# Performance work log

Hardware: AMD Instinct MI355X
Metric: run time of the kernel (lower is better)

Reference implementation:

```python
import jax, jax.numpy as jnp
import numpy as np

H, C = 4, 32          # GAT heads, per-head dim
NH = 4                # transformer heads


def layer_norm(x, g, b, eps=1e-5):
    mu = x.mean(-1, keepdims=True)
    var = ((x - mu) ** 2).mean(-1, keepdims=True)
    return (x - mu) / jnp.sqrt(var + eps) * g + b


def setup_inputs() -> dict:
    key = jax.random.key(0)
    ks = jax.random.split(key, 16)
    B, T, N, F = 256, 72, 5, 10
    D, FF = 128, 256
    # full directed graph on 5 stations, no self loops (E=20)
    ei = np.array([[i, j] for i in range(N) for j in range(N) if i != j], dtype=np.int32).T
    s = 0.1
    return {
        'x': jax.random.normal(ks[0], (B, T, N, F), jnp.float32),
        'edge_index': jnp.asarray(ei),
        'gcn_w': jax.random.normal(ks[1], (F, 64), jnp.float32) * s,
        'gcn_b': jnp.zeros((64,), jnp.float32),
        'gat_w': jax.random.normal(ks[2], (64, H * C), jnp.float32) * s,
        'gat_a_src': jax.random.normal(ks[3], (H, C), jnp.float32) * s,
        'gat_a_dst': jax.random.normal(ks[4], (H, C), jnp.float32) * s,
        'gat_b': jnp.zeros((H * C,), jnp.float32),
        'gln_g': jnp.ones((D,), jnp.float32),
        'gln_b': jnp.zeros((D,), jnp.float32),
        'tw_qkv': jax.random.normal(ks[5], (3, D, 3 * D), jnp.float32) * s,
        'tb_qkv': jnp.zeros((3, 3 * D), jnp.float32),
        'tw_o': jax.random.normal(ks[6], (3, D, D), jnp.float32) * s,
        'tb_o': jnp.zeros((3, D), jnp.float32),
        'ln1_g': jnp.ones((3, D), jnp.float32),
        'ln1_b': jnp.zeros((3, D), jnp.float32),
        'w_ff1': jax.random.normal(ks[7], (3, D, FF), jnp.float32) * s,
        'b_ff1': jnp.zeros((3, FF), jnp.float32),
        'w_ff2': jax.random.normal(ks[8], (3, FF, D), jnp.float32) * s,
        'b_ff2': jnp.zeros((3, D), jnp.float32),
        'ln2_g': jnp.ones((3, D), jnp.float32),
        'ln2_b': jnp.zeros((3, D), jnp.float32),
        'hw1': jax.random.normal(ks[9], (6, D, D // 2), jnp.float32) * s,
        'hb1': jnp.zeros((6, D // 2), jnp.float32),
        'hw2': jax.random.normal(ks[10], (6, D // 2, 5), jnp.float32) * s,
        'hb2': jnp.zeros((6, 5), jnp.float32),
    }


def reference(x, edge_index, gcn_w, gcn_b, gat_w, gat_a_src, gat_a_dst, gat_b,
              gln_g, gln_b, tw_qkv, tb_qkv, tw_o, tb_o, ln1_g, ln1_b,
              w_ff1, b_ff1, w_ff2, b_ff2, ln2_g, ln2_b, hw1, hb1, hw2, hb2):
    B, T, N, F = x.shape
    D = gln_g.shape[0]

    # ---- frozen GCN encoder (torch.no_grad): symmetric-normalized A with self loops
    src, dst = edge_index[0], edge_index[1]
    loop = jnp.arange(N, dtype=src.dtype)
    src2 = jnp.concatenate([src, loop])
    dst2 = jnp.concatenate([dst, loop])
    A = jnp.zeros((N, N), x.dtype).at[dst2, src2].add(1.0)
    deg = A.sum(1)
    dinv = jnp.where(deg > 0, deg ** -0.5, 0.0)
    Anorm = dinv[:, None] * A * dinv[None, :]
    xw = jnp.einsum('btnf,fh->btnh', x, gcn_w) + gcn_b
    gcn = jnp.tanh(jnp.einsum('ij,btjh->btih', Anorm, xw))
    gcn = jax.lax.stop_gradient(gcn)  # encoder is frozen + no_grad

    # ---- GATConv over batched graph (self loops added, PyG default), eval mode (no dropout)
    h = jnp.einsum('btnf,fhc->btnhc', gcn, gat_w.reshape(gcn.shape[-1], H, C))
    a_s = (h * gat_a_src).sum(-1)                         # [B,T,N,H]
    a_d = (h * gat_a_dst).sum(-1)
    e = a_s[:, :, src2, :] + a_d[:, :, dst2, :]           # [B,T,E2,H]
    e = jnp.where(e > 0, e, 0.2 * e)                      # LeakyReLU(0.2)
    eT = jnp.moveaxis(e, 2, 0)                            # [E2,B,T,H]
    m = jax.ops.segment_max(eT, dst2, num_segments=N)
    ex = jnp.exp(eT - m[dst2])
    denom = jax.ops.segment_sum(ex, dst2, num_segments=N)
    alpha = ex / denom[dst2]                              # scatter-softmax per dst node
    hsrc = jnp.moveaxis(h, 2, 0)[src2]                    # [E2,B,T,H,C]
    agg = jax.ops.segment_sum(alpha[..., None] * hsrc, dst2, num_segments=N)
    gat = jnp.moveaxis(agg, 0, 2).reshape(B, T, N, H * C) + gat_b
    gat = layer_norm(gat, gln_g, gln_b)

    # ---- mean-pool stations, positional encoding
    z = gat.mean(2)                                       # [B,T,D]
    pos = jnp.arange(T, dtype=jnp.float32)[:, None]
    div = jnp.exp(jnp.arange(0, D, 2, dtype=jnp.float32) * (-np.log(10000.0) / D))
    pe = jnp.zeros((T, D), x.dtype).at[:, 0::2].set(jnp.sin(pos * div)).at[:, 1::2].set(jnp.cos(pos * div))
    z = z + pe

    # ---- post-norm transformer encoder (relu FF), eval mode
    dh = D // NH
    scale = jnp.sqrt(jnp.asarray(dh, x.dtype))
    for i in range(tw_qkv.shape[0]):
        qkv = z @ tw_qkv[i] + tb_qkv[i]
        q, k, v = jnp.split(qkv, 3, axis=-1)
        q = q.reshape(B, T, NH, dh)
        k = k.reshape(B, T, NH, dh)
        v = v.reshape(B, T, NH, dh)
        att = jax.nn.softmax(jnp.einsum('bqhd,bkhd->bhqk', q, k) / scale, axis=-1)
        o = jnp.einsum('bhqk,bkhd->bqhd', att, v).reshape(B, T, D)
        z = layer_norm(z + o @ tw_o[i] + tb_o[i], ln1_g[i], ln1_b[i])
        ff = jax.nn.relu(z @ w_ff1[i] + b_ff1[i]) @ w_ff2[i] + b_ff2[i]
        z = layer_norm(z + ff, ln2_g[i], ln2_b[i])

    # ---- multi-horizon forecast heads on last timestep -> stacked [6,B,5]
    last = z[:, -1]
    h1 = jax.nn.relu(jnp.einsum('bd,kdm->kbm', last, hw1) + hb1[:, None, :])
    out = jnp.einsum('kbm,kms->kbs', h1, hw2) + hb2[:, None, :]
    return out
```

## Files before the change

### kernel.cpp

```cpp
#include <hip/hip_runtime.h>
#include <hip/hip_bf16.h>

#define B_  256
#define T_  72
#define N_  5
#define F_  10
#define D_  128
#define HH_ 4
#define CC_ 32
#define FF_ 256
#define BT_ (B_*T_)
#define E2MAX 32

#define WS_Z    256
#define WS_QKV  (WS_Z + BT_*D_)
#define WS_OBUF (WS_QKV + BT_*3*D_)
#define WS_WBF  (WS_OBUF + BT_*D_)

#define WOFF_QKV(i)  ((i)*49152)
#define WOFF_O(i)    (147456 + (i)*16384)
#define WOFF_FF1(i)  (196608 + (i)*32768)
#define WOFF_FF2(i)  (294912 + (i)*32768)
#define WOFF_GATW    393216

#define MZF_OFF   0
#define MSB_OFF   38016
#define MSQ_OFF   70784
#define MSK_OFF   92544
#define MVT_OFF   114304
#define MOB_OFF   140928
#define MSMEM_BYTES 162688

typedef __attribute__((ext_vector_type(8))) short bf16x8;
typedef __attribute__((ext_vector_type(4))) float f32x4;

__device__ __forceinline__ unsigned short bf16_rne(float x) {
    unsigned u = __float_as_uint(x);
    unsigned r = (u + 0x7FFFu + ((u >> 16) & 1u)) >> 16;
    return (unsigned short)r;
}
__device__ __forceinline__ unsigned bf16pk(float a, float b) {
    return (unsigned)bf16_rne(a) | ((unsigned)bf16_rne(b) << 16);
}
__device__ __forceinline__ float bf2f(short s) {
    return __uint_as_float(((unsigned)(unsigned short)s) << 16);
}

__global__ void setup_kernel(const int* __restrict__ ei, float* __restrict__ ws, int E) {
    if (threadIdx.x != 0 || blockIdx.x != 0) return;
    int* wsi = (int*)ws;
    const int N = N_;
    int E2 = E + N;
    int src2[E2MAX], dst2[E2MAX];
    for (int e = 0; e < E; ++e) { src2[e] = ei[e]; dst2[e] = ei[E + e]; }
    for (int n = 0; n < N; ++n) { src2[E + n] = n; dst2[E + n] = n; }
    float A[N_ * N_];
    for (int i = 0; i < N * N; ++i) A[i] = 0.f;
    for (int e = 0; e < E2; ++e) A[dst2[e] * N + src2[e]] += 1.f;
    float dinv[N_];
    for (int n = 0; n < N; ++n) {
        float s = 0.f;
        for (int j = 0; j < N; ++j) s += A[n * N + j];
        dinv[n] = (s > 0.f) ? rsqrtf(s) : 0.f;
    }
    for (int n = 0; n < N; ++n)
        for (int j = 0; j < N; ++j)
            ws[n * N + j] = dinv[n] * A[n * N + j] * dinv[j];
    int cnt[N_];
    for (int n = 0; n < N; ++n) cnt[n] = 0;
    for (int e = 0; e < E2; ++e) cnt[dst2[e]]++;
    int off = 0;
    for (int n = 0; n < N; ++n) { wsi[96 + n] = off; off += cnt[n]; }
    wsi[96 + N] = off;
    int cur[N_];
    for (int n = 0; n < N; ++n) cur[n] = wsi[96 + n];
    for (int e = 0; e < E2; ++e) wsi[104 + cur[dst2[e]]++] = e;
    for (int e = 0; e < E2; ++e) { wsi[32 + e] = src2[e]; wsi[64 + e] = dst2[e]; }
}

__global__ __launch_bounds__(256) void prep_kernel(
    const float* __restrict__ tw_qkv, const float* __restrict__ tw_o,
    const float* __restrict__ w_ff1, const float* __restrict__ w_ff2,
    const float* __restrict__ gat_w, short* __restrict__ wbf)
{
    __shared__ float s_t[64][65];
    const int tid = threadIdx.x;
    int t = blockIdx.x;
    const float* src; short* dst; int R, C, tr, tc;
    if (t >= 96) { int q = t - 96; src = gat_w; dst = wbf + WOFF_GATW; R = 64; C = 128; tr = 0; tc = q; }
    else {
        int layer = t / 32, r32 = t % 32;
        if (r32 < 12)      { src = tw_qkv + layer * (128*384); dst = wbf + WOFF_QKV(layer); R = 128; C = 384; tr = r32 / 6;  tc = r32 % 6; }
        else if (r32 < 16) { int q = r32 - 12; src = tw_o + layer * 16384; dst = wbf + WOFF_O(layer);  R = 128; C = 128; tr = q >> 1; tc = q & 1; }
        else if (r32 < 24) { int q = r32 - 16; src = w_ff1 + layer * 32768; dst = wbf + WOFF_FF1(layer); R = 128; C = 256; tr = q >> 2; tc = q & 3; }
        else               { int q = r32 - 24; src = w_ff2 + layer * 32768; dst = wbf + WOFF_FF2(layer); R = 256; C = 128; tr = q >> 1; tc = q & 1; }
    }
    #pragma unroll
    for (int it = 0; it < 16; ++it) {
        int e = it * 256 + tid;
        int r = e >> 6, c = e & 63;
        s_t[r][c] = src[(size_t)(tr*64 + r) * C + tc*64 + c];
    }
    __syncthreads();
    #pragma unroll
    for (int it = 0; it < 16; ++it) {
        int e = it * 256 + tid;
        int c = e >> 6, r = e & 63;
        dst[(size_t)(tc*64 + c) * R + tr*64 + r] = (short)bf16_rne(s_t[r][c]);
    }
}

__device__ __forceinline__ bf16x8 ld_frag(const short* s, int row, int kbase, int ldk) {
    return *(const bf16x8*)&s[row * ldk + (kbase ^ ((row & 7) << 3))];
}

__global__ __launch_bounds__(256) void gcn_h_mfma(
    const float* __restrict__ x, const float* __restrict__ gcn_w, const float* __restrict__ gcn_b,
    const float* __restrict__ a_src, const float* __restrict__ a_dst,
    const float* __restrict__ ws, const short* __restrict__ gwT,
    short* __restrict__ hbuf, float* __restrict__ asb, float* __restrict__ adb)
{
    __shared__ float s_x[16 * 50];
    __shared__ float s_an[25];
    __shared__ short s_gcn[80 * 64];

    const int tid = threadIdx.x;
    const int tok0 = blockIdx.x * 16;

    for (int i = tid; i < 16 * 50; i += 256) s_x[i] = x[(size_t)tok0 * 50 + i];
    if (tid < 25) s_an[tid] = ws[tid];
    __syncthreads();

    #pragma unroll
    for (int it = 0; it < 2; ++it) {
        int idx = it * 256 + tid;
        int tl = idx >> 5, kp = idx & 31;
        int k0 = kp * 2;
        float w0[F_], w1[F_];
        #pragma unroll
        for (int f = 0; f < F_; ++f) { w0[f] = gcn_w[f * 64 + k0]; w1[f] = gcn_w[f * 64 + k0 + 1]; }
        float b0 = gcn_b[k0], b1 = gcn_b[k0 + 1];
        float xw0[N_], xw1[N_];
        #pragma unroll
        for (int n = 0; n < N_; ++n) {
            float a0 = b0, a1 = b1;
            #pragma unroll
            for (int f = 0; f < F_; ++f) {
                float xv = s_x[tl * 50 + n * 10 + f];
                a0 += xv * w0[f]; a1 += xv * w1[f];
            }
            xw0[n] = a0; xw1[n] = a1;
        }
        #pragma unroll
        for (int n = 0; n < N_; ++n) {
            float s0 = 0.f, s1 = 0.f;
            #pragma unroll
            for (int j = 0; j < N_; ++j) { float an = s_an[n * 5 + j]; s0 += an * xw0[j]; s1 += an * xw1[j]; }
            float e0 = __expf(2.f * fabsf(s0)), e1 = __expf(2.f * fabsf(s1));
            float t0 = copysignf(1.f - 2.f / (e0 + 1.f), s0);
            float t1 = copysignf(1.f - 2.f / (e1 + 1.f), s1);
            int row = tl * 5 + n;
            *(unsigned*)&s_gcn[row * 64 + (k0 ^ ((row & 7) << 3))] = bf16pk(t0, t1);
        }
    }
    __syncthreads();

    const int w = tid >> 6, lane = tid & 63;
    const int c = lane & 15, g = lane >> 4;
    const int kf = g * 8;
    bf16x8 bfr[2][2];
    #pragma unroll
    for (int nn = 0; nn < 2; ++nn)
        #pragma unroll
        for (int k0 = 0; k0 < 2; ++k0)
            bfr[nn][k0] = *(const bf16x8*)&gwT[(w * 32 + nn * 16 + c) * 64 + k0 * 32 + kf];
    const float as0 = a_src[w * 32 + c],      as1 = a_src[w * 32 + 16 + c];
    const float ad0 = a_dst[w * 32 + c],      ad1 = a_dst[w * 32 + 16 + c];
    #pragma unroll
    for (int m = 0; m < 5; ++m) {
        bf16x8 af0 = ld_frag(s_gcn, m * 16 + c, kf, 64);
        bf16x8 af1 = ld_frag(s_gcn, m * 16 + c, 32 + kf, 64);
        f32x4 a0 = {0,0,0,0}, a1 = {0,0,0,0};
        a0 = __builtin_amdgcn_mfma_f32_16x16x32_bf16(af0, bfr[0][0], a0, 0, 0, 0);
        a0 = __builtin_amdgcn_mfma_f32_16x16x32_bf16(af1, bfr[0][1], a0, 0, 0, 0);
        a1 = __builtin_amdgcn_mfma_f32_16x16x32_bf16(af0, bfr[1][0], a1, 0, 0, 0);
        a1 = __builtin_amdgcn_mfma_f32_16x16x32_bf16(af1, bfr[1][1], a1, 0, 0, 0);
        float ps[4], pd[4];
        #pragma unroll
        for (int i = 0; i < 4; ++i) {
            int row = m * 16 + g * 4 + i;
            size_t gr = (size_t)(tok0 * 5 + row) * 128;
            hbuf[gr + w * 32 + c]      = (short)bf16_rne(a0[i]);
            hbuf[gr + w * 32 + 16 + c] = (short)bf16_rne(a1[i]);
            ps[i] = a0[i] * as0 + a1[i] * as1;
            pd[i] = a0[i] * ad0 + a1[i] * ad1;
        }
        #pragma unroll
        for (int mm = 1; mm < 16; mm <<= 1)
            #pragma unroll
            for (int i = 0; i < 4; ++i) { ps[i] += __shfl_xor(ps[i], mm); pd[i] += __shfl_xor(pd[i], mm); }
        if (c == 0) {
            #pragma unroll
            for (int i = 0; i < 4; ++i) {
                int row = m * 16 + g * 4 + i;
                asb[(size_t)(tok0 * 5 + row) * 4 + w] = ps[i];
                adb[(size_t)(tok0 * 5 + row) * 4 + w] = pd[i];
            }
        }
    }
}

__global__ __launch_bounds__(256) void gat_agg(
    const short* __restrict__ hbuf, const float* __restrict__ asb, const float* __restrict__ adb,
    const float* __restrict__ gat_b, const float* __restrict__ gln_g, const float* __restrict__ gln_b,
    const float* __restrict__ ws, float* __restrict__ z, int E2)
{
    __shared__ int   s_src[E2MAX], s_csr_off[N_ + 1], s_csr_e[E2MAX];
    __shared__ float s_alpha[4][E2MAX][4];
    __shared__ short s_h[4 * 5 * 128];
    __shared__ float s_asl[4][N_][4], s_adl[4][N_][4];

    const int tid = threadIdx.x;
    const int wv = tid >> 6, lane = tid & 63;
    const int tok = blockIdx.x * 4 + wv;
    const int* wsi = (const int*)ws;

    if (tid < E2) { s_src[tid] = wsi[32 + tid]; s_csr_e[tid] = wsi[104 + tid]; }
    if (tid < N_ + 1) s_csr_off[tid] = wsi[96 + tid];
    if (tid >= 64 && tid < 144) ((float*)s_asl)[tid - 64] = asb[(size_t)blockIdx.x * 80 + tid - 64];
    if (tid >= 144 && tid < 224) ((float*)s_adl)[tid - 144] = adb[(size_t)blockIdx.x * 80 + tid - 144];
    {
        const uint4* hb4 = (const uint4*)(hbuf + (size_t)blockIdx.x * 4 * 5 * 128);
        uint4* sh4 = (uint4*)s_h;
        #pragma unroll
        for (int it = 0; it < 2; ++it) {
            int i = it * 256 + tid;
            if (i < 320) sh4[i] = hb4[i];
        }
    }
    __syncthreads();

    if (lane < 20) {
        int dn = lane >> 2, head = lane & 3;
        int j0 = s_csr_off[dn], j1 = s_csr_off[dn + 1];
        float adv = s_adl[wv][dn][head];
        float mx = -1e30f;
        for (int j = j0; j < j1; ++j) {
            int e = s_csr_e[j];
            float ev = s_asl[wv][s_src[e]][head] + adv;
            ev = ev > 0.f ? ev : 0.2f * ev;
            mx = fmaxf(mx, ev);
        }
        float den = 0.f;
        for (int j = j0; j < j1; ++j) {
            int e = s_csr_e[j];
            float ev = s_asl[wv][s_src[e]][head] + adv;
            ev = ev > 0.f ? ev : 0.2f * ev;
            float ex = __expf(ev - mx);
            den += ex;
            s_alpha[wv][e][head] = ex;
        }
        float r = 1.f / den;
        for (int j = j0; j < j1; ++j) s_alpha[wv][s_csr_e[j]][head] *= r;
    }
    __syncthreads();

    const int h0 = lane >> 5, h1 = 2 + (lane >> 5);
    const float gb0 = gat_b[lane],      gb1 = gat_b[lane + 64];
    const float gg0 = gln_g[lane],      gg1 = gln_g[lane + 64];
    const float gB0 = gln_b[lane],      gB1 = gln_b[lane + 64];
    float v0[N_], v1[N_];
    #pragma unroll
    for (int n = 0; n < N_; ++n) {
        float a0 = 0.f, a1 = 0.f;
        int j0 = s_csr_off[n], j1 = s_csr_off[n + 1];
        for (int j = j0; j < j1; ++j) {
            int e = s_csr_e[j];
            int rb = (wv * 5 + s_src[e]) * 128;
            a0 += s_alpha[wv][e][h0] * bf2f(s_h[rb + lane]);
            a1 += s_alpha[wv][e][h1] * bf2f(s_h[rb + lane + 64]);
        }
        v0[n] = a0 + gb0; v1[n] = a1 + gb1;
    }
    float r1[N_], r2[N_];
    #pragma unroll
    for (int n = 0; n < N_; ++n) { r1[n] = v0[n] + v1[n]; r2[n] = v0[n]*v0[n] + v1[n]*v1[n]; }
    #pragma unroll
    for (int mm = 1; mm < 64; mm <<= 1)
        #pragma unroll
        for (int n = 0; n < N_; ++n) { r1[n] += __shfl_xor(r1[n], mm); r2[n] += __shfl_xor(r2[n], mm); }
    float z0 = 0.f, z1 = 0.f;
    #pragma unroll
    for (int n = 0; n < N_; ++n) {
        float mu = r1[n] * (1.f / D_);
        float var = r2[n] * (1.f / D_) - mu * mu;
        float rstd = rsqrtf(var + 1e-5f);
        z0 += (v0[n] - mu) * rstd * gg0 + gB0;
        z1 += (v1[n] - mu) * rstd * gg1 + gB1;
    }
    z0 *= (1.f / N_); z1 *= (1.f / N_);
    const float cpe = -9.210340371976184f / (float)D_;
    int t = tok % T_;
    float dv0 = __expf((float)(lane & ~1) * cpe);
    float dv1 = __expf((float)((lane + 64) & ~1) * cpe);
    float ang0 = (float)t * dv0, ang1 = (float)t * dv1;
    z0 += (lane & 1) ? __cosf(ang0) : __sinf(ang0);
    z1 += (lane & 1) ? __cosf(ang1) : __sinf(ang1);
    z[(size_t)tok * D_ + lane] = z0;
    z[(size_t)tok * D_ + 64 + lane] = z1;
}

__global__ __launch_bounds__(512, 1) void layers_fused(
    const float* __restrict__ zg, const short* __restrict__ wbf,
    const float* __restrict__ tb_qkv, const float* __restrict__ tb_o,
    const float* __restrict__ ln1_g, const float* __restrict__ ln1_b,
    const float* __restrict__ b_ff1, const float* __restrict__ b_ff2,
    const float* __restrict__ ln2_g, const float* __restrict__ ln2_b,
    const float* __restrict__ hw1, const float* __restrict__ hb1,
    const float* __restrict__ hw2, const float* __restrict__ hb2,
    float* __restrict__ out)
{
    extern __shared__ char smem[];
    float* s_zf = (float*)(smem + MZF_OFF);
    short* s_b  = (short*)(smem + MSB_OFF);
    short* s_q  = (short*)(smem + MSQ_OFF);
    short* s_k  = (short*)(smem + MSK_OFF);
    short* s_vt = (short*)(smem + MVT_OFF);
    short* s_ob = (short*)(smem + MOB_OFF);
    short* s_f  = s_q;
    short* s_z1 = s_vt;

    const int tid = threadIdx.x;
    const int w = tid >> 6, lane = tid & 63;
    const int c = lane & 15, g = lane >> 4;
    const int kf = g * 8;
    const int b = blockIdx.x;

    for (int idx = tid; idx < 72 * 64; idx += 512) {
        int r = idx >> 6, c2 = (idx & 63) * 2;
        float2 v = *(const float2*)&zg[(size_t)(b * T_ + r) * D_ + c2];
        s_zf[r * 132 + c2]     = v.x;
        s_zf[r * 132 + c2 + 1] = v.y;
        *(unsigned*)&s_b[r * 136 + c2] = bf16pk(v.x, v.y);
    }
    {
        int r = 72 + (tid >> 6), cc = (tid & 63) * 2;
        *(unsigned*)&s_b[r * 136 + cc] = 0;
    }
    for (int idx = tid; idx < 128 * 16; idx += 512) {
        int chn = idx >> 4, key = 72 + (idx & 15) * 2;
        *(unsigned*)&s_vt[chn * 104 + key] = 0;
    }
    __syncthreads();

    for (int L = 0; L < 3; ++L) {
        const short* Wq = wbf + WOFF_QKV(L);
        const short* Wo = wbf + WOFF_O(L);
        const short* W1 = wbf + WOFF_FF1(L);
        const short* W2 = wbf + WOFF_FF2(L);
        const float* bq = tb_qkv + L * 384;
        const float* bo = tb_o + L * D_;
        const float* g1 = ln1_g + L * D_, *be1 = ln1_b + L * D_;
        const float* b1 = b_ff1 + L * FF_, *b2 = b_ff2 + L * D_;
        const float* g2 = ln2_g + L * D_, *be2 = ln2_b + L * D_;

        {
            const int wcol = w * 16 + c;
            bf16x8 Bf[3][4];
            float bv[3];
            #pragma unroll
            for (int ch = 0; ch < 3; ++ch) {
                const short* Wc = Wq + (size_t)(ch * 128 + wcol) * 128;
                #pragma unroll
                for (int k0 = 0; k0 < 4; ++k0) Bf[ch][k0] = *(const bf16x8*)&Wc[k0 * 32 + kf];
                bv[ch] = bq[ch * 128 + wcol];
            }
            #pragma unroll
            for (int m = 0; m < 5; ++m) {
                bf16x8 Af[4];
                #pragma unroll
                for (int k0 = 0; k0 < 4; ++k0)
                    Af[k0] = *(const bf16x8*)&s_b[(m * 16 + c) * 136 + k0 * 32 + kf];
                f32x4 aq = {bv[0], bv[0], bv[0], bv[0]};
                f32x4 ak = {bv[1], bv[1], bv[1], bv[1]};
                f32x4 av = {bv[2], bv[2], bv[2], bv[2]};
                #pragma unroll
                for (int k0 = 0; k0 < 4; ++k0) {
                    aq = __builtin_amdgcn_mfma_f32_16x16x32_bf16(Af[k0], Bf[0][k0], aq, 0, 0, 0);
                    ak = __builtin_amdgcn_mfma_f32_16x16x32_bf16(Af[k0], Bf[1][k0], ak, 0, 0, 0);
                    av = __builtin_amdgcn_mfma_f32_16x16x32_bf16(Af[k0], Bf[2][k0], av, 0, 0, 0);
                }
                #pragma unroll
                for (int i = 0; i < 4; ++i) {
                    int lrow = m * 16 + g * 4 + i;
                    s_q[lrow * 136 + wcol]  = (short)bf16_rne(aq[i]);
                    s_k[lrow * 136 + wcol]  = (short)bf16_rne(ak[i]);
                    s_vt[wcol * 104 + lrow] = (short)bf16_rne(av[i]);
                }
            }
        }
        __syncthreads();

        {
            short* pstrip = s_b + w * (16 * 104);
            for (int t2 = lane; t2 < 16 * 24; t2 += 64) {
                int r = t2 / 24, col = 80 + (t2 % 24);
                pstrip[r * 104 + col] = 0;
            }
            const int h = w & 3;
            const int mlo = (w >> 2) ? 3 : 0;
            const int mhi = (w >> 2) ? 5 : 3;
            const float scale = 0.17677669529663687f;
            for (int m = mlo; m < mhi; ++m) {
                bf16x8 aq = *(const bf16x8*)&s_q[(m * 16 + c) * 136 + h * 32 + kf];
                float ps[5][4], mx[4], den[4];
                #pragma unroll
                for (int i = 0; i < 4; ++i) mx[i] = -1e30f;
                #pragma unroll
                for (int n0 = 0; n0 < 5; ++n0) {
                    bf16x8 bk = *(const bf16x8*)&s_k[(n0 * 16 + c) * 136 + h * 32 + kf];
                    f32x4 z4 = {0,0,0,0};
                    f32x4 accS = __builtin_amdgcn_mfma_f32_16x16x32_bf16(aq, bk, z4, 0, 0, 0);
                    #pragma unroll
                    for (int i = 0; i < 4; ++i) {
                        float s = accS[i] * scale;
                        if (n0 == 4 && c >= 8) s = -1e30f;
                        ps[n0][i] = s;
                        mx[i] = fmaxf(mx[i], s);
                    }
                }
                #pragma unroll
                for (int mm = 1; mm < 16; mm <<= 1)
                    #pragma unroll
                    for (int i = 0; i < 4; ++i) mx[i] = fmaxf(mx[i], __shfl_xor(mx[i], mm));
                #pragma unroll
                for (int i = 0; i < 4; ++i) den[i] = 0.f;
                #pragma unroll
                for (int n0 = 0; n0 < 5; ++n0)
                    #pragma unroll
                    for (int i = 0; i < 4; ++i) { float e = __expf(ps[n0][i] - mx[i]); ps[n0][i] = e; den[i] += e; }
                #pragma unroll
                for (int mm = 1; mm < 16; mm <<= 1)
                    #pragma unroll
                    for (int i = 0; i < 4; ++i) den[i] += __shfl_xor(den[i], mm);
                float rden[4];
                #pragma unroll
                for (int i = 0; i < 4; ++i) rden[i] = 1.f / den[i];
                #pragma unroll
                for (int n0 = 0; n0 < 5; ++n0)
                    #pragma unroll
                    for (int i = 0; i < 4; ++i)
                        pstrip[(g * 4 + i) * 104 + n0 * 16 + c] = (short)bf16_rne(ps[n0][i] * rden[i]);
                f32x4 accO[2] = {{0,0,0,0},{0,0,0,0}};
                #pragma unroll
                for (int kt = 0; kt < 3; ++kt) {
                    bf16x8 ap = *(const bf16x8*)&pstrip[c * 104 + kt * 32 + kf];
                    #pragma unroll
                    for (int n0 = 0; n0 < 2; ++n0) {
                        bf16x8 bv = *(const bf16x8*)&s_vt[(h * 32 + n0 * 16 + c) * 104 + kt * 32 + kf];
                        accO[n0] = __builtin_amdgcn_mfma_f32_16x16x32_bf16(ap, bv, accO[n0], 0, 0, 0);
                    }
                }
                #pragma unroll
                for (int n0 = 0; n0 < 2; ++n0)
                    #pragma unroll
                    for (int i = 0; i < 4; ++i)
                        s_ob[(m * 16 + g * 4 + i) * 136 + h * 32 + n0 * 16 + c] = (short)bf16_rne(accO[n0][i]);
            }
        }
        __syncthreads();

        if (w < 5) {
            const int m = w;
            bf16x8 Af[4];
            #pragma unroll
            for (int k0 = 0; k0 < 4; ++k0)
                Af[k0] = *(const bf16x8*)&s_ob[(m * 16 + c) * 136 + k0 * 32 + kf];
            f32x4 acc[8];
            #pragma unroll
            for (int n0 = 0; n0 < 8; ++n0) {
                const short* Wp = Wo + (size_t)(n0 * 16 + c) * 128;
                float bvv = bo[n0 * 16 + c];
                f32x4 a = {bvv, bvv, bvv, bvv};
                #pragma unroll
                for (int k0 = 0; k0 < 4; ++k0) {
                    bf16x8 bfg = *(const bf16x8*)&Wp[k0 * 32 + kf];
                    a = __builtin_amdgcn_mfma_f32_16x16x32_bf16(Af[k0], bfg, a, 0, 0, 0);
                }
                acc[n0] = a;
            }
            #pragma unroll
            for (int n0 = 0; n0 < 8; ++n0)
                #pragma unroll
                for (int i = 0; i < 4; ++i) {
                    int row = m * 16 + g * 4 + i;
                    acc[n0][i] += (row < 72) ? s_zf[row * 132 + n0 * 16 + c] : 0.f;
                }
            float s1[4] = {0,0,0,0}, s2[4] = {0,0,0,0};
            #pragma unroll
            for (int n0 = 0; n0 < 8; ++n0)
                #pragma unroll
                for (int i = 0; i < 4; ++i) { float v = acc[n0][i]; s1[i] += v; s2[i] += v * v; }
            #pragma unroll
            for (int mm = 1; mm < 16; mm <<= 1)
                #pragma unroll
                for (int i = 0; i < 4; ++i) { s1[i] += __shfl_xor(s1[i], mm); s2[i] += __shfl_xor(s2[i], mm); }
            #pragma unroll
            for (int i = 0; i < 4; ++i) {
                float mu = s1[i] * (1.f / D_);
                float var = s2[i] * (1.f / D_) - mu * mu;
                float rstd = rsqrtf(var + 1e-5f);
                int row = m * 16 + g * 4 + i;
                #pragma unroll
                for (int n0 = 0; n0 < 8; ++n0) {
                    float v = (acc[n0][i] - mu) * rstd * g1[n0 * 16 + c] + be1[n0 * 16 + c];
                    if (row < 72) s_zf[row * 132 + n0 * 16 + c] = v;
                    s_z1[row * 136 + n0 * 16 + c] = (short)bf16_rne(v);
                }
            }
        }
        __syncthreads();

        {
            const int wcol = w * 16 + c;
            #pragma unroll
            for (int ch = 0; ch < 2; ++ch) {
                const short* Wp = W1 + (size_t)(ch * 128 + wcol) * 128;
                bf16x8 Bf[4];
                #pragma unroll
                for (int k0 = 0; k0 < 4; ++k0) Bf[k0] = *(const bf16x8*)&Wp[k0 * 32 + kf];
                const float bvv = b1[ch * 128 + wcol];
                #pragma unroll
                for (int m = 0; m < 5; ++m) {
                    bf16x8 Af[4];
                    #pragma unroll
                    for (int k0 = 0; k0 < 4; ++k0)
                        Af[k0] = *(const bf16x8*)&s_z1[(m * 16 + c) * 136 + k0 * 32 + kf];
                    f32x4 a = {bvv, bvv, bvv, bvv};
                    #pragma unroll
                    for (int k0 = 0; k0 < 4; ++k0)
                        a = __builtin_amdgcn_mfma_f32_16x16x32_bf16(Af[k0], Bf[k0], a, 0, 0, 0);
                    #pragma unroll
                    for (int i = 0; i < 4; ++i) {
                        int lrow = m * 16 + g * 4 + i;
                        s_f[lrow * 264 + ch * 128 + wcol] = (short)bf16_rne(fmaxf(a[i], 0.f));
                    }
                }
            }
        }
        __syncthreads();

        if (w < 5) {
            const int m = w;
            f32x4 acc2[8];
            #pragma unroll
            for (int n0 = 0; n0 < 8; ++n0) {
                float bvv = b2[n0 * 16 + c];
                acc2[n0] = (f32x4){bvv, bvv, bvv, bvv};
            }
            #pragma unroll
            for (int kc = 0; kc < 2; ++kc) {
                bf16x8 Af[4];
                #pragma unroll
                for (int k0 = 0; k0 < 4; ++k0)
                    Af[k0] = *(const bf16x8*)&s_f[(m * 16 + c) * 264 + kc * 128 + k0 * 32 + kf];
                #pragma unroll
                for (int n0 = 0; n0 < 8; ++n0) {
                    const short* Wp = W2 + (size_t)(n0 * 16 + c) * 256 + kc * 128;
                    #pragma unroll
                    for (int k0 = 0; k0 < 4; ++k0) {
                        bf16x8 bfg = *(const bf16x8*)&Wp[k0 * 32 + kf];
                        acc2[n0] = __builtin_amdgcn_mfma_f32_16x16x32_bf16(Af[k0], bfg, acc2[n0], 0, 0, 0);
                    }
                }
            }
            #pragma unroll
            for (int n0 = 0; n0 < 8; ++n0)
                #pragma unroll
                for (int i = 0; i < 4; ++i) {
                    int row = m * 16 + g * 4 + i;
                    acc2[n0][i] += (row < 72) ? s_zf[row * 132 + n0 * 16 + c] : 0.f;
                }
            float s1[4] = {0,0,0,0}, s2[4] = {0,0,0,0};
            #pragma unroll
            for (int n0 = 0; n0 < 8; ++n0)
                #pragma unroll
                for (int i = 0; i < 4; ++i) { float v = acc2[n0][i]; s1[i] += v; s2[i] += v * v; }
            #pragma unroll
            for (int mm = 1; mm < 16; mm <<= 1)
                #pragma unroll
                for (int i = 0; i < 4; ++i) { s1[i] += __shfl_xor(s1[i], mm); s2[i] += __shfl_xor(s2[i], mm); }
            #pragma unroll
            for (int i = 0; i < 4; ++i) {
                float mu = s1[i] * (1.f / D_);
                float var = s2[i] * (1.f / D_) - mu * mu;
                float rstd = rsqrtf(var + 1e-5f);
                int row = m * 16 + g * 4 + i;
                if (row < 72) {
                    #pragma unroll
                    for (int n0 = 0; n0 < 8; ++n0) {
                        float v = (acc2[n0][i] - mu) * rstd * g2[n0 * 16 + c] + be2[n0 * 16 + c];
                        s_zf[row * 132 + n0 * 16 + c] = v;
                        s_b[row * 136 + n0 * 16 + c] = (short)bf16_rne(v);
                    }
                }
            }
        } else {
            int wl = (w - 5) * 64 + lane;
            for (int i = wl; i < 512; i += 192) {
                int r = 72 + (i >> 6), cc = (i & 63) * 2;
                *(unsigned*)&s_b[r * 136 + cc] = 0;
            }
        }
        __syncthreads();
    }

    float* s_h1 = (float*)s_b;
    for (int t2 = tid; t2 < 384; t2 += 512) {
        int k = t2 >> 6, j = t2 & 63;
        float acc = hb1[k * 64 + j];
        const float* w1p = hw1 + (size_t)k * D_ * 64 + j;
        for (int d = 0; d < D_; ++d) acc += s_zf[71 * 132 + d] * w1p[d * 64];
        s_h1[k * 64 + j] = fmaxf(acc, 0.f);
    }
    __syncthreads();
    if (tid < 30) {
        int k = tid / 5, s = tid % 5;
        float o = hb2[k * 5 + s];
        const float* w2p = hw2 + (size_t)k * 64 * 5 + s;
        for (int j = 0; j < 64; ++j) o += s_h1[k * 64 + j] * w2p[j * 5];
        out[(size_t)k * (B_ * 5) + b * 5 + s] = o;
    }
}

extern "C" void kernel_launch(void* const* d_in, const int* in_sizes, int n_in,
                              void* d_out, int out_size, void* d_ws, size_t ws_size,
                              hipStream_t stream) {
    const float* x      = (const float*)d_in[0];
    const int*   ei     = (const int*)  d_in[1];
    const float* gcn_w  = (const float*)d_in[2];
    const float* gcn_b  = (const float*)d_in[3];
    const float* gat_w  = (const float*)d_in[4];
    const float* a_src  = (const float*)d_in[5];
    const float* a_dst  = (const float*)d_in[6];
    const float* gat_b  = (const float*)d_in[7];
    const float* gln_g  = (const float*)d_in[8];
    const float* gln_b  = (const float*)d_in[9];
    const float* tw_qkv = (const float*)d_in[10];
    const float* tb_qkv = (const float*)d_in[11];
    const float* tw_o   = (const float*)d_in[12];
    const float* tb_o   = (const float*)d_in[13];
    const float* ln1_g  = (const float*)d_in[14];
    const float* ln1_b  = (const float*)d_in[15];
    const float* w_ff1  = (const float*)d_in[16];
    const float* b_ff1  = (const float*)d_in[17];
    const float* w_ff2  = (const float*)d_in[18];
    const float* b_ff2  = (const float*)d_in[19];
    const float* ln2_g  = (const float*)d_in[20];
    const float* ln2_b  = (const float*)d_in[21];
    const float* hw1    = (const float*)d_in[22];
    const float* hb1    = (const float*)d_in[23];
    const float* hw2    = (const float*)d_in[24];
    const float* hb2    = (const float*)d_in[25];
    float* out = (float*)d_out;
    float* ws  = (float*)d_ws;

    float* z   = ws + WS_Z;
    short* wbf = (short*)(ws + WS_WBF);

    short* hbuf = (short*)(ws + WS_QKV);
    float* asb  = ws + WS_OBUF;
    float* adb  = ws + WS_OBUF + BT_ * 5 * 4;

    const int E = in_sizes[1] / 2;
    const int E2 = E + N_;

    static bool attr_set = false;
    if (!attr_set) {
        hipFuncSetAttribute((const void*)layers_fused,
                            hipFuncAttributeMaxDynamicSharedMemorySize, MSMEM_BYTES);
        attr_set = true;
    }

    setup_kernel<<<1, 64, 0, stream>>>(ei, ws, E);
    prep_kernel<<<98, 256, 0, stream>>>(tw_qkv, tw_o, w_ff1, w_ff2, gat_w, wbf);
    gcn_h_mfma<<<BT_ / 16, 256, 0, stream>>>(x, gcn_w, gcn_b, a_src, a_dst, ws,
                                             wbf + WOFF_GATW, hbuf, asb, adb);
    gat_agg<<<BT_ / 4, 256, 0, stream>>>(hbuf, asb, adb, gat_b, gln_g, gln_b, ws, z, E2);
    layers_fused<<<B_, 512, MSMEM_BYTES, stream>>>(z, wbf, tb_qkv, tb_o,
                                                   ln1_g, ln1_b, b_ff1, b_ff2,
                                                   ln2_g, ln2_b, hw1, hb1, hw2, hb2, out);
}
```

Baseline: 287.0 us.

## Double fused-layer block to 1024 threads and split GEMM/LayerNorm work across more waves

The fused transformer kernel now launches 1024 threads (16 waves) per batch element instead of 512. The QKV, FF1, out-projection and FF2 stages are split across twice as many waves. LayerNorm row statistics are combined through a shared-memory scratch column, which needs an extra barrier per LayerNorm. The goal is more latency hiding and shorter per-wave serial MFMA chains, since with 256 blocks each CU had only one 8-wave block. The cost is more synchronisation, tighter register limits at 1024 threads, and idle waves during attention.

```diff
diff --git a/kernel.cpp b/kernel.cpp
--- a/kernel.cpp
+++ b/kernel.cpp
@@ -310,7 +310,7 @@
     z[(size_t)tok * D_ + 64 + lane] = z1;
 }
 
-__global__ __launch_bounds__(512, 1) void layers_fused(
+__global__ __launch_bounds__(1024, 1) void layers_fused(
     const float* __restrict__ zg, const short* __restrict__ wbf,
     const float* __restrict__ tb_qkv, const float* __restrict__ tb_o,
     const float* __restrict__ ln1_g, const float* __restrict__ ln1_b,
@@ -336,18 +336,18 @@
     const int kf = g * 8;
     const int b = blockIdx.x;
 
-    for (int idx = tid; idx < 72 * 64; idx += 512) {
+    for (int idx = tid; idx < 72 * 64; idx += 1024) {
         int r = idx >> 6, c2 = (idx & 63) * 2;
         float2 v = *(const float2*)&zg[(size_t)(b * T_ + r) * D_ + c2];
         s_zf[r * 132 + c2]     = v.x;
         s_zf[r * 132 + c2 + 1] = v.y;
         *(unsigned*)&s_b[r * 136 + c2] = bf16pk(v.x, v.y);
     }
-    {
+    if (tid < 512) {
         int r = 72 + (tid >> 6), cc = (tid & 63) * 2;
         *(unsigned*)&s_b[r * 136 + cc] = 0;
     }
-    for (int idx = tid; idx < 128 * 16; idx += 512) {
+    for (int idx = tid; idx < 128 * 16; idx += 1024) {
         int chn = idx >> 4, key = 72 + (idx & 15) * 2;
         *(unsigned*)&s_vt[chn * 104 + key] = 0;
     }
@@ -365,7 +365,9 @@
         const float* g2 = ln2_g + L * D_, *be2 = ln2_b + L * D_;
 
         {
-            const int wcol = w * 16 + c;
+            const int wcol = (w & 7) * 16 + c;
+            const int mlo = (w >> 3) ? 3 : 0;
+            const int mhi = (w >> 3) ? 5 : 3;
             bf16x8 Bf[3][4];
             float bv[3];
             #pragma unroll
@@ -375,8 +377,7 @@
                 for (int k0 = 0; k0 < 4; ++k0) Bf[ch][k0] = *(const bf16x8*)&Wc[k0 * 32 + kf];
                 bv[ch] = bq[ch * 128 + wcol];
             }
-            #pragma unroll
-            for (int m = 0; m < 5; ++m) {
+            for (int m = mlo; m < mhi; ++m) {
                 bf16x8 Af[4];
                 #pragma unroll
                 for (int k0 = 0; k0 < 4; ++k0)
@@ -401,7 +402,7 @@
         }
         __syncthreads();
 
-        {
+        if (w < 8) {
             short* pstrip = s_b + w * (16 * 104);
             for (int t2 = lane; t2 < 16 * 24; t2 += 64) {
                 int r = t2 / 24, col = 80 + (t2 % 24);
@@ -470,15 +471,16 @@
         }
         __syncthreads();
 
-        if (w < 5) {
-            const int m = w;
+        f32x4 acc[4];
+        if (w < 10) {
+            const int m = w >> 1, hf = w & 1;
             bf16x8 Af[4];
             #pragma unroll
             for (int k0 = 0; k0 < 4; ++k0)
                 Af[k0] = *(const bf16x8*)&s_ob[(m * 16 + c) * 136 + k0 * 32 + kf];
-            f32x4 acc[8];
-            #pragma unroll
-            for (int n0 = 0; n0 < 8; ++n0) {
+            #pragma unroll
+            for (int n0r = 0; n0r < 4; ++n0r) {
+                const int n0 = hf * 4 + n0r;
                 const short* Wp = Wo + (size_t)(n0 * 16 + c) * 128;
                 float bvv = bo[n0 * 16 + c];
                 f32x4 a = {bvv, bvv, bvv, bvv};
@@ -487,76 +489,93 @@
                     bf16x8 bfg = *(const bf16x8*)&Wp[k0 * 32 + kf];
                     a = __builtin_amdgcn_mfma_f32_16x16x32_bf16(Af[k0], bfg, a, 0, 0, 0);
                 }
-                acc[n0] = a;
-            }
-            #pragma unroll
-            for (int n0 = 0; n0 < 8; ++n0)
+                acc[n0r] = a;
+            }
+            #pragma unroll
+            for (int n0r = 0; n0r < 4; ++n0r)
                 #pragma unroll
                 for (int i = 0; i < 4; ++i) {
                     int row = m * 16 + g * 4 + i;
-                    acc[n0][i] += (row < 72) ? s_zf[row * 132 + n0 * 16 + c] : 0.f;
+                    acc[n0r][i] += (row < 72) ? s_zf[row * 132 + (hf * 4 + n0r) * 16 + c] : 0.f;
                 }
             float s1[4] = {0,0,0,0}, s2[4] = {0,0,0,0};
             #pragma unroll
-            for (int n0 = 0; n0 < 8; ++n0)
-                #pragma unroll
-                for (int i = 0; i < 4; ++i) { float v = acc[n0][i]; s1[i] += v; s2[i] += v * v; }
+            for (int n0r = 0; n0r < 4; ++n0r)
+                #pragma unroll
+                for (int i = 0; i < 4; ++i) { float v = acc[n0r][i]; s1[i] += v; s2[i] += v * v; }
             #pragma unroll
             for (int mm = 1; mm < 16; mm <<= 1)
                 #pragma unroll
                 for (int i = 0; i < 4; ++i) { s1[i] += __shfl_xor(s1[i], mm); s2[i] += __shfl_xor(s2[i], mm); }
+            if (c == 0) {
+                #pragma unroll
+                for (int i = 0; i < 4; ++i) {
+                    int row = m * 16 + g * 4 + i;
+                    if (row < 72) {
+                        s_zf[row * 132 + 128 + hf * 2]     = s1[i];
+                        s_zf[row * 132 + 128 + hf * 2 + 1] = s2[i];
+                    }
+                }
+            }
+        }
+        __syncthreads();
+        if (w < 10) {
+            const int m = w >> 1, hf = w & 1;
             #pragma unroll
             for (int i = 0; i < 4; ++i) {
-                float mu = s1[i] * (1.f / D_);
-                float var = s2[i] * (1.f / D_) - mu * mu;
-                float rstd = rsqrtf(var + 1e-5f);
                 int row = m * 16 + g * 4 + i;
-                #pragma unroll
-                for (int n0 = 0; n0 < 8; ++n0) {
-                    float v = (acc[n0][i] - mu) * rstd * g1[n0 * 16 + c] + be1[n0 * 16 + c];
-                    if (row < 72) s_zf[row * 132 + n0 * 16 + c] = v;
-                    s_z1[row * 136 + n0 * 16 + c] = (short)bf16_rne(v);
+                if (row < 72) {
+                    float s1t = s_zf[row * 132 + 128] + s_zf[row * 132 + 130];
+                    float s2t = s_zf[row * 132 + 129] + s_zf[row * 132 + 131];
+                    float mu = s1t * (1.f / D_);
+                    float var = s2t * (1.f / D_) - mu * mu;
+                    float rstd = rsqrtf(var + 1e-5f);
+                    #pragma unroll
+                    for (int n0r = 0; n0r < 4; ++n0r) {
+                        int col = (hf * 4 + n0r) * 16 + c;
+                        float v = (acc[n0r][i] - mu) * rstd * g1[col] + be1[col];
+                        s_zf[row * 132 + col] = v;
+                        s_z1[row * 136 + col] = (short)bf16_rne(v);
+                    }
                 }
             }
         }
         __syncthreads();
 
         {
-            const int wcol = w * 16 + c;
-            #pragma unroll
-            for (int ch = 0; ch < 2; ++ch) {
-                const short* Wp = W1 + (size_t)(ch * 128 + wcol) * 128;
-                bf16x8 Bf[4];
-                #pragma unroll
-                for (int k0 = 0; k0 < 4; ++k0) Bf[k0] = *(const bf16x8*)&Wp[k0 * 32 + kf];
-                const float bvv = b1[ch * 128 + wcol];
-                #pragma unroll
-                for (int m = 0; m < 5; ++m) {
-                    bf16x8 Af[4];
-                    #pragma unroll
-                    for (int k0 = 0; k0 < 4; ++k0)
-                        Af[k0] = *(const bf16x8*)&s_z1[(m * 16 + c) * 136 + k0 * 32 + kf];
-                    f32x4 a = {bvv, bvv, bvv, bvv};
-                    #pragma unroll
-                    for (int k0 = 0; k0 < 4; ++k0)
-                        a = __builtin_amdgcn_mfma_f32_16x16x32_bf16(Af[k0], Bf[k0], a, 0, 0, 0);
-                    #pragma unroll
-                    for (int i = 0; i < 4; ++i) {
-                        int lrow = m * 16 + g * 4 + i;
-                        s_f[lrow * 264 + ch * 128 + wcol] = (short)bf16_rne(fmaxf(a[i], 0.f));
-                    }
+            const int ch = w >> 3;
+            const int wcol = (w & 7) * 16 + c;
+            const short* Wp = W1 + (size_t)(ch * 128 + wcol) * 128;
+            bf16x8 Bf[4];
+            #pragma unroll
+            for (int k0 = 0; k0 < 4; ++k0) Bf[k0] = *(const bf16x8*)&Wp[k0 * 32 + kf];
+            const float bvv = b1[ch * 128 + wcol];
+            #pragma unroll
+            for (int m = 0; m < 5; ++m) {
+                bf16x8 Af[4];
+                #pragma unroll
+                for (int k0 = 0; k0 < 4; ++k0)
+                    Af[k0] = *(const bf16x8*)&s_z1[(m * 16 + c) * 136 + k0 * 32 + kf];
+                f32x4 a = {bvv, bvv, bvv, bvv};
+                #pragma unroll
+                for (int k0 = 0; k0 < 4; ++k0)
+                    a = __builtin_amdgcn_mfma_f32_16x16x32_bf16(Af[k0], Bf[k0], a, 0, 0, 0);
+                #pragma unroll
+                for (int i = 0; i < 4; ++i) {
+                    int lrow = m * 16 + g * 4 + i;
+                    s_f[lrow * 264 + ch * 128 + wcol] = (short)bf16_rne(fmaxf(a[i], 0.f));
                 }
             }
         }
         __syncthreads();
 
-        if (w < 5) {
-            const int m = w;
-            f32x4 acc2[8];
-            #pragma unroll
-            for (int n0 = 0; n0 < 8; ++n0) {
-                float bvv = b2[n0 * 16 + c];
-                acc2[n0] = (f32x4){bvv, bvv, bvv, bvv};
+        f32x4 acc2[4];
+        if (w < 10) {
+            const int m = w >> 1, hf = w & 1;
+            #pragma unroll
+            for (int n0r = 0; n0r < 4; ++n0r) {
+                float bvv = b2[(hf * 4 + n0r) * 16 + c];
+                acc2[n0r] = (f32x4){bvv, bvv, bvv, bvv};
             }
             #pragma unroll
             for (int kc = 0; kc < 2; ++kc) {
@@ -565,59 +584,76 @@
                 for (int k0 = 0; k0 < 4; ++k0)
                     Af[k0] = *(const bf16x8*)&s_f[(m * 16 + c) * 264 + kc * 128 + k0 * 32 + kf];
                 #pragma unroll
-                for (int n0 = 0; n0 < 8; ++n0) {
-                    const short* Wp = W2 + (size_t)(n0 * 16 + c) * 256 + kc * 128;
+                for (int n0r = 0; n0r < 4; ++n0r) {
+                    const short* Wp = W2 + (size_t)((hf * 4 + n0r) * 16 + c) * 256 + kc * 128;
                     #pragma unroll
                     for (int k0 = 0; k0 < 4; ++k0) {
                         bf16x8 bfg = *(const bf16x8*)&Wp[k0 * 32 + kf];
-                        acc2[n0] = __builtin_amdgcn_mfma_f32_16x16x32_bf16(Af[k0], bfg, acc2[n0], 0, 0, 0);
+                        acc2[n0r] = __builtin_amdgcn_mfma_f32_16x16x32_bf16(Af[k0], bfg, acc2[n0r], 0, 0, 0);
                     }
                 }
             }
             #pragma unroll
-            for (int n0 = 0; n0 < 8; ++n0)
+            for (int n0r = 0; n0r < 4; ++n0r)
                 #pragma unroll
                 for (int i = 0; i < 4; ++i) {
                     int row = m * 16 + g * 4 + i;
-                    acc2[n0][i] += (row < 72) ? s_zf[row * 132 + n0 * 16 + c] : 0.f;
+                    acc2[n0r][i] += (row < 72) ? s_zf[row * 132 + (hf * 4 + n0r) * 16 + c] : 0.f;
                 }
             float s1[4] = {0,0,0,0}, s2[4] = {0,0,0,0};
             #pragma unroll
-            for (int n0 = 0; n0 < 8; ++n0)
-                #pragma unroll
-                for (int i = 0; i < 4; ++i) { float v = acc2[n0][i]; s1[i] += v; s2[i] += v * v; }
+            for (int n0r = 0; n0r < 4; ++n0r)
+                #pragma unroll
+                for (int i = 0; i < 4; ++i) { float v = acc2[n0r][i]; s1[i] += v; s2[i] += v * v; }
             #pragma unroll
             for (int mm = 1; mm < 16; mm <<= 1)
                 #pragma unroll
                 for (int i = 0; i < 4; ++i) { s1[i] += __shfl_xor(s1[i], mm); s2[i] += __shfl_xor(s2[i], mm); }
+            if (c == 0) {
+                #pragma unroll
+                for (int i = 0; i < 4; ++i) {
+                    int row = m * 16 + g * 4 + i;
+                    if (row < 72) {
+                        s_zf[row * 132 + 128 + hf * 2]     = s1[i];
+                        s_zf[row * 132 + 128 + hf * 2 + 1] = s2[i];
+                    }
+                }
+            }
+        } else {
+            int wl = (w - 10) * 64 + lane;
+            for (int i = wl; i < 512; i += 384) {
+                int r = 72 + (i >> 6), cc = (i & 63) * 2;
+                *(unsigned*)&s_b[r * 136 + cc] = 0;
+            }
+        }
+        __syncthreads();
+        if (w < 10) {
+            const int m = w >> 1, hf = w & 1;
             #pragma unroll
             for (int i = 0; i < 4; ++i) {
-                float mu = s1[i] * (1.f / D_);
-                float var = s2[i] * (1.f / D_) - mu * mu;
-                float rstd = rsqrtf(var + 1e-5f);
                 int row = m * 16 + g * 4 + i;
                 if (row < 72) {
-                    #pragma unroll
-                    for (int n0 = 0; n0 < 8; ++n0) {
-                        float v = (acc2[n0][i] - mu) * rstd * g2[n0 * 16 + c] + be2[n0 * 16 + c];
-                        s_zf[row * 132 + n0 * 16 + c] = v;
-                        s_b[row * 136 + n0 * 16 + c] = (short)bf16_rne(v);
+                    float s1t = s_zf[row * 132 + 128] + s_zf[row * 132 + 130];
+                    float s2t = s_zf[row * 132 + 129] + s_zf[row * 132 + 131];
+                    float mu = s1t * (1.f / D_);
+                    float var = s2t * (1.f / D_) - mu * mu;
+                    float rstd = rsqrtf(var + 1e-5f);
+                    #pragma unroll
+                    for (int n0r = 0; n0r < 4; ++n0r) {
+                        int col = (hf * 4 + n0r) * 16 + c;
+                        float v = (acc2[n0r][i] - mu) * rstd * g2[col] + be2[col];
+                        s_zf[row * 132 + col] = v;
+                        s_b[row * 136 + col] = (short)bf16_rne(v);
                     }
                 }
             }
-        } else {
-            int wl = (w - 5) * 64 + lane;
-            for (int i = wl; i < 512; i += 192) {
-                int r = 72 + (i >> 6), cc = (i & 63) * 2;
-                *(unsigned*)&s_b[r * 136 + cc] = 0;
-            }
         }
         __syncthreads();
     }
 
     float* s_h1 = (float*)s_b;
-    for (int t2 = tid; t2 < 384; t2 += 512) {
-        int k = t2 >> 6, j = t2 & 63;
+    if (tid < 384) {
+        int k = tid >> 6, j = tid & 63;
         float acc = hb1[k * 64 + j];
         const float* w1p = hw1 + (size_t)k * D_ * 64 + j;
         for (int d = 0; d < D_; ++d) acc += s_zf[71 * 132 + d] * w1p[d * 64];
@@ -687,7 +723,7 @@
     gcn_h_mfma<<<BT_ / 16, 256, 0, stream>>>(x, gcn_w, gcn_b, a_src, a_dst, ws,
                                              wbf + WOFF_GATW, hbuf, asb, adb);
     gat_agg<<<BT_ / 4, 256, 0, stream>>>(hbuf, asb, adb, gat_b, gln_g, gln_b, ws, z, E2);
-    layers_fused<<<B_, 512, MSMEM_BYTES, stream>>>(z, wbf, tb_qkv, tb_o,
-                                                   ln1_g, ln1_b, b_ff1, b_ff2,
-                                                   ln2_g, ln2_b, hw1, hb1, hw2, hb2, out);
-}
+    layers_fused<<<B_, 1024, MSMEM_BYTES, stream>>>(z, wbf, tb_qkv, tb_o,
+                                                    ln1_g, ln1_b, b_ff1, b_ff2,
+                                                    ln2_g, ln2_b, hw1, hb1, hw2, hb2, out);
+}
```

New measurement: 361.8 us. +26.0%, slower.
